# Kernel tuning notes

Hardware: AMD Instinct MI355X
Metric: run time of the kernel (lower is better)

The kernel has to match this reference:

```python
import jax, jax.numpy as jnp
import numpy as np

N = 100000
IN_DIM = 256
HID = 128
E = 1600000


def setup_inputs() -> dict:
    key = jax.random.key(0)
    ks = jax.random.split(key, 6)
    x = jax.random.normal(ks[0], (N, IN_DIM), dtype=jnp.float32)
    edge_index = jax.random.randint(ks[1], (2, E), 0, N, dtype=jnp.int64)
    # GCNConv weight (hidden, in) and bias (hidden); decoder Linear (in, hidden) + bias
    s_in = 1.0 / np.sqrt(IN_DIM)
    s_h = 1.0 / np.sqrt(HID)
    W_enc = jax.random.uniform(ks[2], (HID, IN_DIM), jnp.float32, -s_in, s_in)
    b_enc = jnp.zeros((HID,), jnp.float32)
    W_dec = jax.random.uniform(ks[3], (IN_DIM, HID), jnp.float32, -s_h, s_h)
    b_dec = jax.random.uniform(ks[4], (IN_DIM,), jnp.float32, -s_h, s_h)
    return {"x": x, "edge_index": edge_index, "W_enc": W_enc, "b_enc": b_enc,
            "W_dec": W_dec, "b_dec": b_dec}


def gcn_conv(x, edge_index, W, b):
    # Linear transform first (PyG GCNConv): h = x @ W^T  -> [N, HID]
    h = x @ W.T
    # Add self-loops
    loops = jnp.arange(N, dtype=edge_index.dtype)
    row = jnp.concatenate([edge_index[0], loops])  # source
    col = jnp.concatenate([edge_index[1], loops])  # target
    # Symmetric normalization: deg over targets (incl. self-loops)
    deg = jax.ops.segment_sum(jnp.ones_like(col, dtype=h.dtype), col, num_segments=N)
    dinv = jax.lax.rsqrt(deg)  # deg >= 1 due to self-loops
    norm = dinv[row] * dinv[col]  # [E+N]
    msg = h[row] * norm[:, None]  # gather + scale  [E+N, HID]
    agg = jax.ops.segment_sum(msg, col, num_segments=N)  # scatter-add
    return agg + b


def reference(x, edge_index, W_enc, b_enc, W_dec, b_dec):
    z = jax.nn.relu(gcn_conv(x, edge_index, W_enc, b_enc))
    x_recon = z @ W_dec.T + b_dec
    return (z, x_recon)
```

## Files before the change

### kernel.cpp

```cpp
#include <hip/hip_runtime.h>
#include <hip/hip_bf16.h>

#define NDIM 256
#define HDIM 128
#define NPAD 100352
#define LDS1_STRIDE 264
#define LDS2_STRIDE 136
#define P2CAP 6144

typedef __bf16 bf16_t;
typedef bf16_t bf16x2 __attribute__((ext_vector_type(2)));
typedef bf16_t bf16x4 __attribute__((ext_vector_type(4)));
typedef bf16_t bf16x8 __attribute__((ext_vector_type(8)));
typedef float f32x2 __attribute__((ext_vector_type(2)));
typedef float f32x4 __attribute__((ext_vector_type(4)));

__device__ __forceinline__ float bflo(unsigned u) { return __uint_as_float(u << 16); }
__device__ __forceinline__ float bfhi(unsigned u) { return __uint_as_float(u & 0xffff0000u); }

__global__ __launch_bounds__(256) void k_prep(const float* __restrict__ We, bf16_t* __restrict__ wpe,
                                              const float* __restrict__ Wd, bf16_t* __restrict__ wpd) {
    const int b = blockIdx.x, t = threadIdx.x;
    const bool enc = b < 16;
    const int i = (enc ? b : b - 16) * 256 + t;
    const int lane = i & 63;
    const int fr = lane & 15, kg = lane >> 4;
    int nf, kk32, K, NF;
    const float* W;
    bf16_t* wp;
    if (enc) { nf = (i >> 6) & 7;  kk32 = i >> 9;  K = NDIM; NF = 8;  W = We; wp = wpe; }
    else     { nf = (i >> 6) & 15; kk32 = i >> 10; K = HDIM; NF = 16; W = Wd; wp = wpd; }
    const float* src = &W[(size_t)(nf * 16 + fr) * K + kk32 * 32 + kg * 8];
    const f32x4 a0 = *reinterpret_cast<const f32x4*>(src);
    const f32x4 a1 = *reinterpret_cast<const f32x4*>(src + 4);
    bf16x8 o;
    o[0] = (bf16_t)a0[0]; o[1] = (bf16_t)a0[1]; o[2] = (bf16_t)a0[2]; o[3] = (bf16_t)a0[3];
    o[4] = (bf16_t)a1[0]; o[5] = (bf16_t)a1[1]; o[6] = (bf16_t)a1[2]; o[7] = (bf16_t)a1[3];
    reinterpret_cast<bf16x8*>(wp)[(kk32 * NF + nf) * 64 + lane] = o;
}

template<int K, int NC, bool OUT_BF16>
__device__ __forceinline__ void mfma_epi(const bf16x8* af,
                                         const bf16_t* __restrict__ Wp,
                                         const float* __restrict__ bias,
                                         void* __restrict__ Cout,
                                         const int bid, const int nrows) {
    const int lane = threadIdx.x & 63;
    const int wv = threadIdx.x >> 6;
    const int fr = lane & 15;
    const int kg = lane >> 4;
    constexpr int NF = NC / 16, NK = K / 32;

    const bf16x8* wp = reinterpret_cast<const bf16x8*>(Wp);
    f32x4 acc[NF];
    const f32x4 zero4 = {0.f, 0.f, 0.f, 0.f};
    #pragma unroll
    for (int nf = 0; nf < NF; ++nf) acc[nf] = zero4;

    #pragma unroll
    for (int k = 0; k < NK; ++k) {
        #pragma unroll
        for (int nf = 0; nf < NF; ++nf)
            acc[nf] = __builtin_amdgcn_mfma_f32_16x16x32_bf16(af[k], wp[(k * NF + nf) * 64 + lane], acc[nf], 0, 0, 0);
    }

    const long long rbase = (long long)bid * 64 + wv * 16 + kg * 4;
    #pragma unroll
    for (int nf = 0; nf < NF; ++nf) {
        const int c = nf * 16 + fr;
        const float bv = bias ? bias[c] : 0.f;
        #pragma unroll
        for (int i = 0; i < 4; ++i) {
            const long long r = rbase + i;
            if (r < nrows) {
                const float v = acc[nf][i] + bv;
                if (OUT_BF16) ((bf16_t*)Cout)[r * NC + c] = (bf16_t)v;
                else          __builtin_nontemporal_store(v, &((float*)Cout)[r * NC + c]);
            }
        }
    }
}

__device__ __forceinline__ void gemm1_body(const int bid, const float* __restrict__ x,
                                           const bf16_t* __restrict__ wpe,
                                           bf16_t* __restrict__ hb, const int nrows,
                                           bf16_t* lds) {
    const int t = threadIdx.x;
    const long long rowbase = (long long)bid * 64;
    #pragma unroll
    for (int p = 0; p < 16; ++p) {
        const int s = p * 256 + t;
        const int r = s >> 6, c4 = s & 63;
        long long gr = rowbase + r;
        if (gr >= nrows) gr = nrows - 1;
        const f32x4 v = __builtin_nontemporal_load(reinterpret_cast<const f32x4*>(&x[gr * NDIM + c4 * 4]));
        bf16x4 o;
        o[0] = (bf16_t)v[0]; o[1] = (bf16_t)v[1]; o[2] = (bf16_t)v[2]; o[3] = (bf16_t)v[3];
        *reinterpret_cast<bf16x4*>(&lds[r * LDS1_STRIDE + c4 * 4]) = o;
    }
    __syncthreads();
    const int lane = t & 63, wv = t >> 6, fr = lane & 15, kg = lane >> 4;
    bf16x8 af[8];
    #pragma unroll
    for (int k = 0; k < 8; ++k)
        af[k] = *reinterpret_cast<const bf16x8*>(&lds[(wv * 16 + fr) * LDS1_STRIDE + k * 32 + kg * 8]);
    mfma_epi<NDIM, HDIM, true>(af, wpe, nullptr, hb, bid, nrows);
}

__device__ __forceinline__ void p1a_body(const int blk, const int* __restrict__ col,
                                         int* __restrict__ bcnt, const int E_,
                                         const int nbkt, const int epb, int* lhist) {
    const int t = threadIdx.x;
    for (int i = t; i < nbkt; i += 256) lhist[i] = 0;
    __syncthreads();
    const int base = blk * epb;
    const int cnt = min(E_ - base, epb);
    for (int i = t; i < cnt; i += 256)
        atomicAdd(&lhist[col[base + i] >> 8], 1);
    __syncthreads();
    for (int i = t; i < nbkt; i += 256)
        bcnt[i * 256 + blk] = lhist[i];
}

__global__ __launch_bounds__(256) void k_fused(const float* __restrict__ x,
                                               const bf16_t* __restrict__ wpe,
                                               bf16_t* __restrict__ hb, const int nrows,
                                               const int* __restrict__ col,
                                               int* __restrict__ bcnt,
                                               const int E_, const int nbkt, const int epb,
                                               const int G1) {
    __shared__ __align__(16) bf16_t lds[64 * LDS1_STRIDE];
    const int b = blockIdx.x;
    if (b < G1) gemm1_body(b, x, wpe, hb, nrows, lds);
    else        p1a_body(b - G1, col, bcnt, E_, nbkt, epb, (int*)lds);
}

__global__ __launch_bounds__(256) void k_scanB1(const int* __restrict__ bcnt,
                                                int* __restrict__ bsum, const int M) {
    __shared__ int s[256];
    const int b = blockIdx.x, t = threadIdx.x;
    const int i0 = b * 1024 + t * 4;
    int4 v = make_int4(0, 0, 0, 0);
    if (i0 + 4 <= M) v = *reinterpret_cast<const int4*>(&bcnt[i0]);
    else if (i0 < M) {
        const int k = M - i0;
        v.x = bcnt[i0];
        if (k > 1) v.y = bcnt[i0 + 1];
        if (k > 2) v.z = bcnt[i0 + 2];
    }
    s[t] = v.x + v.y + v.z + v.w;
    __syncthreads();
    for (int d = 128; d > 0; d >>= 1) {
        if (t < d) s[t] += s[t + d];
        __syncthreads();
    }
    if (t == 0) bsum[b] = s[0];
}

__global__ __launch_bounds__(128) void k_scanB2(const int* __restrict__ bsum,
                                                int* __restrict__ bofs,
                                                int* __restrict__ bbase,
                                                const int nb, const int M) {
    __shared__ int s[128];
    const int t = threadIdx.x;
    const int v = (t < nb) ? bsum[t] : 0;
    s[t] = v;
    __syncthreads();
    for (int d = 1; d < 128; d <<= 1) {
        int xx = (t >= d) ? s[t - d] : 0;
        __syncthreads();
        s[t] += xx;
        __syncthreads();
    }
    if (t < nb) bofs[t] = s[t] - v;
    if (t == nb - 1) bbase[M] = s[t];
}

__global__ __launch_bounds__(256) void k_scanB3(const int* __restrict__ bcnt,
                                                const int* __restrict__ bofs,
                                                int* __restrict__ bbase, const int M) {
    __shared__ int s[256];
    const int b = blockIdx.x, t = threadIdx.x;
    const int i0 = b * 1024 + t * 4;
    int4 v = make_int4(0, 0, 0, 0);
    if (i0 + 4 <= M) v = *reinterpret_cast<const int4*>(&bcnt[i0]);
    else if (i0 < M) {
        const int k = M - i0;
        v.x = bcnt[i0];
        if (k > 1) v.y = bcnt[i0 + 1];
        if (k > 2) v.z = bcnt[i0 + 2];
    }
    const int tsum = v.x + v.y + v.z + v.w;
    s[t] = tsum;
    __syncthreads();
    for (int d = 1; d < 256; d <<= 1) {
        int xx = (t >= d) ? s[t - d] : 0;
        __syncthreads();
        s[t] += xx;
        __syncthreads();
    }
    const int excl = s[t] - tsum + bofs[b];
    int4 o;
    o.x = excl; o.y = excl + v.x; o.z = o.y + v.y; o.w = o.z + v.z;
    if (i0 + 4 <= M) *reinterpret_cast<int4*>(&bbase[i0]) = o;
    else if (i0 < M) {
        const int k = M - i0;
        bbase[i0] = o.x;
        if (k > 1) bbase[i0 + 1] = o.y;
        if (k > 2) bbase[i0 + 2] = o.z;
    }
}

__global__ __launch_bounds__(256) void k_p1b(const int* __restrict__ row,
                                             const int* __restrict__ col,
                                             const int* __restrict__ bbase,
                                             int* __restrict__ pbuf,
                                             const int E_, const int nbkt, const int epb) {
    __shared__ int lcur[512];
    const int blk = blockIdx.x, t = threadIdx.x;
    for (int i = t; i < nbkt; i += 256) lcur[i] = bbase[i * 256 + blk];
    __syncthreads();
    const int base = blk * epb;
    const int cnt = min(E_ - base, epb);
    for (int i = t; i < cnt; i += 256) {
        const int c = col[base + i];
        const int r = row[base + i];
        const int pos = atomicAdd(&lcur[c >> 8], 1);
        pbuf[pos] = r | ((c & 255) << 17);
    }
}

__global__ __launch_bounds__(256) void k_p2(const int* __restrict__ pbuf,
                                            const int* __restrict__ bbase,
                                            int* __restrict__ ebuf,
                                            int* __restrict__ goff, int* __restrict__ gcnt,
                                            float* __restrict__ dinv,
                                            unsigned* __restrict__ hbw,
                                            const int n, const int E_) {
    __shared__ int lcnt[256], lscan[256], lcur[256];
    __shared__ float ldinv[256];
    __shared__ __align__(16) int ecache[P2CAP];
    const int b = blockIdx.x, t = threadIdx.x;
    const int start = bbase[b * 256];
    const int end = bbase[(b + 1) * 256];
    const int size = end - start;
    const bool inlds = size <= P2CAP;
    lcnt[t] = 0; lcur[t] = 0;
    __syncthreads();
    if (inlds) {
        for (int i = t; i < size; i += 256) {
            const int e = pbuf[start + i];
            ecache[i] = e;
            atomicAdd(&lcnt[(e >> 17) & 255], 1);
        }
    } else {
        for (int i = t; i < size; i += 256)
            atomicAdd(&lcnt[(pbuf[start + i] >> 17) & 255], 1);
    }
    __syncthreads();
    const int v = lcnt[t];
    lscan[t] = v;
    __syncthreads();
    for (int d = 1; d < 256; d <<= 1) {
        int xx = (t >= d) ? lscan[t - d] : 0;
        __syncthreads();
        lscan[t] += xx;
        __syncthreads();
    }
    const int excl = lscan[t] - v;
    const int node = (b << 8) + t;
    float dvv = 0.f;
    if (node < n) {
        dvv = rsqrtf((float)(v + 1));
        goff[node] = start + excl;
        gcnt[node] = v;
        dinv[node] = dvv;
    }
    ldinv[t] = dvv;
    lscan[t] = excl;
    __syncthreads();
    for (int i = t; i < size; i += 256) {
        const int e = inlds ? ecache[i] : pbuf[start + i];
        const int li = (e >> 17) & 255;
        const int rk = atomicAdd(&lcur[li], 1);
        ebuf[start + lscan[li] + rk] = e & 0x1FFFF;
    }
    const int wv = t >> 6, lane = t & 63;
    #pragma unroll 4
    for (int rr = wv * 64; rr < wv * 64 + 64; ++rr) {
        const int nd = (b << 8) + rr;
        if (nd >= n) break;
        const float dv = ldinv[rr];
        unsigned* p = &hbw[(size_t)nd * 64 + lane];
        const unsigned u = *p;
        bf16x2 pk;
        pk[0] = (bf16_t)(bflo(u) * dv);
        pk[1] = (bf16_t)(bfhi(u) * dv);
        *p = __builtin_bit_cast(unsigned, pk);
    }
}

__global__ __launch_bounds__(256) void k_agg(const int* __restrict__ ebuf,
                                             const int* __restrict__ off,
                                             const int* __restrict__ cnt,
                                             const float* __restrict__ dinv,
                                             const unsigned* __restrict__ hb,
                                             const float* __restrict__ benc,
                                             float* __restrict__ z,
                                             bf16_t* __restrict__ zb, int n) {
    const int node = blockIdx.x * 4 + (threadIdx.x >> 6);
    const int lane = threadIdx.x & 63;
    if (node >= n) return;
    const float dc = dinv[node];
    const unsigned hself = hb[(size_t)node * 64 + lane];
    float acc0 = bflo(hself);
    float acc1 = bfhi(hself);
    const int base = off[node], m = cnt[node];
    int j = 0;
    for (; j + 16 <= m; j += 16) {
        int r[16]; unsigned u[16];
        #pragma unroll
        for (int q = 0; q < 16; ++q) r[q] = ebuf[base + j + q];
        #pragma unroll
        for (int q = 0; q < 16; ++q) u[q] = hb[(size_t)r[q] * 64 + lane];
        #pragma unroll
        for (int q = 0; q < 16; ++q) {
            acc0 += bflo(u[q]);
            acc1 += bfhi(u[q]);
        }
    }
    for (; j + 4 <= m; j += 4) {
        int r[4]; unsigned u[4];
        #pragma unroll
        for (int q = 0; q < 4; ++q) r[q] = ebuf[base + j + q];
        #pragma unroll
        for (int q = 0; q < 4; ++q) u[q] = hb[(size_t)r[q] * 64 + lane];
        #pragma unroll
        for (int q = 0; q < 4; ++q) {
            acc0 += bflo(u[q]);
            acc1 += bfhi(u[q]);
        }
    }
    for (; j < m; ++j) {
        const unsigned u = hb[(size_t)ebuf[base + j] * 64 + lane];
        acc0 += bflo(u);
        acc1 += bfhi(u);
    }
    f32x2 o;
    o[0] = fmaxf(fmaf(dc, acc0, benc[lane * 2]), 0.f);
    o[1] = fmaxf(fmaf(dc, acc1, benc[lane * 2 + 1]), 0.f);
    *reinterpret_cast<f32x2*>(&z[(size_t)node * HDIM + lane * 2]) = o;
    bf16x2 ob;
    ob[0] = (bf16_t)o[0];
    ob[1] = (bf16_t)o[1];
    *reinterpret_cast<bf16x2*>(&zb[(size_t)node * HDIM + lane * 2]) = ob;
}

__global__ __launch_bounds__(256) void k_gemm2(const bf16_t* __restrict__ zb,
                                               const bf16_t* __restrict__ wpd,
                                               const float* __restrict__ bias,
                                               float* __restrict__ xrec, const int nrows) {
    __shared__ __align__(16) bf16_t lds[64 * LDS2_STRIDE];
    const int t = threadIdx.x;
    const long long rowbase = (long long)blockIdx.x * 64;
    #pragma unroll
    for (int p = 0; p < 4; ++p) {
        const int s = p * 256 + t;
        const int r = s >> 4, c8 = s & 15;
        long long gr = rowbase + r;
        if (gr >= nrows) gr = nrows - 1;
        const bf16x8 v = *reinterpret_cast<const bf16x8*>(&zb[gr * HDIM + c8 * 8]);
        *reinterpret_cast<bf16x8*>(&lds[r * LDS2_STRIDE + c8 * 8]) = v;
    }
    __syncthreads();
    const int lane = t & 63, wv = t >> 6, fr = lane & 15, kg = lane >> 4;
    bf16x8 af[4];
    #pragma unroll
    for (int k = 0; k < 4; ++k)
        af[k] = *reinterpret_cast<const bf16x8*>(&lds[(wv * 16 + fr) * LDS2_STRIDE + k * 32 + kg * 8]);
    mfma_epi<HDIM, NDIM, false>(af, wpd, bias, xrec, blockIdx.x, nrows);
}

extern "C" void kernel_launch(void* const* d_in, const int* in_sizes, int n_in,
                              void* d_out, int out_size, void* d_ws, size_t ws_size,
                              hipStream_t stream) {
    const float* x     = (const float*)d_in[0];
    const int*   ei    = (const int*)d_in[1];
    const float* W_enc = (const float*)d_in[2];
    const float* b_enc = (const float*)d_in[3];
    const float* W_dec = (const float*)d_in[4];
    const float* b_dec = (const float*)d_in[5];

    const int N = in_sizes[0] / NDIM;
    const int E = in_sizes[1] / 2;
    const int* row = ei;
    const int* col = ei + E;

    const int NBKT = (N + 255) >> 8;
    const int M = NBKT * 256;
    const int EPB = (E + 255) / 256;
    const int G1 = (N + 63) / 64;
    const int SB = (M + 1023) / 1024;

    char* wsp = (char*)d_ws;
    int*    pbuf = (int*)wsp;
    bf16_t* zb   = (bf16_t*)wsp;
    const size_t r0 = ((size_t)N * HDIM * 2 > (size_t)E * 4) ? (size_t)N * HDIM * 2 : (size_t)E * 4;
    bf16_t* hb   = (bf16_t*)(wsp + r0);
    int*    ebuf = (int*)(wsp + r0 + (size_t)N * HDIM * 2);
    int*    goff = ebuf + E;
    int*    gcnt = goff + NPAD;
    float*  dinv = (float*)(gcnt + NPAD);
    int*    bcnt = (int*)(dinv + NPAD);
    int*    bbase = bcnt + M;
    int*    bsum = bbase + M + 1;
    int*    bofs = bsum + 128;
    bf16_t* wpe  = (bf16_t*)(bofs + 128);
    bf16_t* wpd  = wpe + HDIM * NDIM;

    float* z    = (float*)d_out;
    float* xrec = (float*)d_out + (size_t)N * HDIM;

    k_prep<<<32, 256, 0, stream>>>(W_enc, wpe, W_dec, wpd);

    k_fused<<<G1 + 256, 256, 0, stream>>>(x, wpe, hb, N, col, bcnt, E, NBKT, EPB, G1);

    k_scanB1<<<SB, 256, 0, stream>>>(bcnt, bsum, M);
    k_scanB2<<<1, 128, 0, stream>>>(bsum, bofs, bbase, SB, M);
    k_scanB3<<<SB, 256, 0, stream>>>(bcnt, bofs, bbase, M);

    k_p1b<<<256, 256, 0, stream>>>(row, col, bbase, pbuf, E, NBKT, EPB);

    k_p2<<<NBKT, 256, 0, stream>>>(pbuf, bbase, ebuf, goff, gcnt, dinv, (unsigned*)hb, N, E);

    k_agg<<<(N + 3) / 4, 256, 0, stream>>>(ebuf, goff, gcnt, dinv, (const unsigned*)hb, b_enc, z, zb, N);

    k_gemm2<<<G1, 256, 0, stream>>>(zb, wpd, b_dec, xrec, N);
}
```

Measured before the change: 224.1 us.

## Fuse neighbor aggregation with decoder GEMM via LDS staging of z tile

Measured after the change: 276.0 us. 1.23x slower.

```diff
diff --git a/kernel.cpp b/kernel.cpp
--- a/kernel.cpp
+++ b/kernel.cpp
@@ -300,85 +300,79 @@
     }
 }
 
-__global__ __launch_bounds__(256) void k_agg(const int* __restrict__ ebuf,
-                                             const int* __restrict__ off,
-                                             const int* __restrict__ cnt,
-                                             const float* __restrict__ dinv,
-                                             const unsigned* __restrict__ hb,
-                                             const float* __restrict__ benc,
-                                             float* __restrict__ z,
-                                             bf16_t* __restrict__ zb, int n) {
-    const int node = blockIdx.x * 4 + (threadIdx.x >> 6);
-    const int lane = threadIdx.x & 63;
-    if (node >= n) return;
-    const float dc = dinv[node];
-    const unsigned hself = hb[(size_t)node * 64 + lane];
-    float acc0 = bflo(hself);
-    float acc1 = bfhi(hself);
-    const int base = off[node], m = cnt[node];
-    int j = 0;
-    for (; j + 16 <= m; j += 16) {
-        int r[16]; unsigned u[16];
-        #pragma unroll
-        for (int q = 0; q < 16; ++q) r[q] = ebuf[base + j + q];
-        #pragma unroll
-        for (int q = 0; q < 16; ++q) u[q] = hb[(size_t)r[q] * 64 + lane];
-        #pragma unroll
-        for (int q = 0; q < 16; ++q) {
-            acc0 += bflo(u[q]);
-            acc1 += bfhi(u[q]);
-        }
-    }
-    for (; j + 4 <= m; j += 4) {
-        int r[4]; unsigned u[4];
-        #pragma unroll
-        for (int q = 0; q < 4; ++q) r[q] = ebuf[base + j + q];
-        #pragma unroll
-        for (int q = 0; q < 4; ++q) u[q] = hb[(size_t)r[q] * 64 + lane];
-        #pragma unroll
-        for (int q = 0; q < 4; ++q) {
-            acc0 += bflo(u[q]);
-            acc1 += bfhi(u[q]);
-        }
-    }
-    for (; j < m; ++j) {
-        const unsigned u = hb[(size_t)ebuf[base + j] * 64 + lane];
-        acc0 += bflo(u);
-        acc1 += bfhi(u);
-    }
-    f32x2 o;
-    o[0] = fmaxf(fmaf(dc, acc0, benc[lane * 2]), 0.f);
-    o[1] = fmaxf(fmaf(dc, acc1, benc[lane * 2 + 1]), 0.f);
-    *reinterpret_cast<f32x2*>(&z[(size_t)node * HDIM + lane * 2]) = o;
-    bf16x2 ob;
-    ob[0] = (bf16_t)o[0];
-    ob[1] = (bf16_t)o[1];
-    *reinterpret_cast<bf16x2*>(&zb[(size_t)node * HDIM + lane * 2]) = ob;
-}
-
-__global__ __launch_bounds__(256) void k_gemm2(const bf16_t* __restrict__ zb,
-                                               const bf16_t* __restrict__ wpd,
-                                               const float* __restrict__ bias,
-                                               float* __restrict__ xrec, const int nrows) {
+__global__ __launch_bounds__(256) void k_aggdec(const int* __restrict__ ebuf,
+                                                const int* __restrict__ off,
+                                                const int* __restrict__ cnt,
+                                                const float* __restrict__ dinv,
+                                                const unsigned* __restrict__ hb,
+                                                const float* __restrict__ benc,
+                                                const bf16_t* __restrict__ wpd,
+                                                const float* __restrict__ bdec,
+                                                float* __restrict__ z,
+                                                float* __restrict__ xrec, int n) {
     __shared__ __align__(16) bf16_t lds[64 * LDS2_STRIDE];
     const int t = threadIdx.x;
-    const long long rowbase = (long long)blockIdx.x * 64;
-    #pragma unroll
-    for (int p = 0; p < 4; ++p) {
-        const int s = p * 256 + t;
-        const int r = s >> 4, c8 = s & 15;
-        long long gr = rowbase + r;
-        if (gr >= nrows) gr = nrows - 1;
-        const bf16x8 v = *reinterpret_cast<const bf16x8*>(&zb[gr * HDIM + c8 * 8]);
-        *reinterpret_cast<bf16x8*>(&lds[r * LDS2_STRIDE + c8 * 8]) = v;
-    }
-    __syncthreads();
-    const int lane = t & 63, wv = t >> 6, fr = lane & 15, kg = lane >> 4;
+    const int wv = t >> 6, lane = t & 63;
+    const int nodebase = blockIdx.x * 64 + wv * 16;
+
+    for (int i = 0; i < 16; ++i) {
+        const int node = nodebase + i;
+        float acc0 = 0.f, acc1 = 0.f;
+        float dc = 0.f;
+        if (node < n) {
+            dc = dinv[node];
+            const unsigned hself = hb[(size_t)node * 64 + lane];
+            acc0 = bflo(hself);
+            acc1 = bfhi(hself);
+            const int base = off[node], m = cnt[node];
+            int j = 0;
+            for (; j + 16 <= m; j += 16) {
+                int r[16]; unsigned u[16];
+                #pragma unroll
+                for (int q = 0; q < 16; ++q) r[q] = ebuf[base + j + q];
+                #pragma unroll
+                for (int q = 0; q < 16; ++q) u[q] = hb[(size_t)r[q] * 64 + lane];
+                #pragma unroll
+                for (int q = 0; q < 16; ++q) {
+                    acc0 += bflo(u[q]);
+                    acc1 += bfhi(u[q]);
+                }
+            }
+            for (; j + 4 <= m; j += 4) {
+                int r[4]; unsigned u[4];
+                #pragma unroll
+                for (int q = 0; q < 4; ++q) r[q] = ebuf[base + j + q];
+                #pragma unroll
+                for (int q = 0; q < 4; ++q) u[q] = hb[(size_t)r[q] * 64 + lane];
+                #pragma unroll
+                for (int q = 0; q < 4; ++q) {
+                    acc0 += bflo(u[q]);
+                    acc1 += bfhi(u[q]);
+                }
+            }
+            for (; j < m; ++j) {
+                const unsigned u = hb[(size_t)ebuf[base + j] * 64 + lane];
+                acc0 += bflo(u);
+                acc1 += bfhi(u);
+            }
+        }
+        f32x2 o;
+        o[0] = fmaxf(fmaf(dc, acc0, benc[lane * 2]), 0.f);
+        o[1] = fmaxf(fmaf(dc, acc1, benc[lane * 2 + 1]), 0.f);
+        if (node < n)
+            *reinterpret_cast<f32x2*>(&z[(size_t)node * HDIM + lane * 2]) = o;
+        bf16x2 ob;
+        ob[0] = (node < n) ? (bf16_t)o[0] : (bf16_t)0.f;
+        ob[1] = (node < n) ? (bf16_t)o[1] : (bf16_t)0.f;
+        *reinterpret_cast<bf16x2*>(&lds[(wv * 16 + i) * LDS2_STRIDE + lane * 2]) = ob;
+    }
+
+    const int fr = lane & 15, kg = lane >> 4;
     bf16x8 af[4];
     #pragma unroll
     for (int k = 0; k < 4; ++k)
         af[k] = *reinterpret_cast<const bf16x8*>(&lds[(wv * 16 + fr) * LDS2_STRIDE + k * 32 + kg * 8]);
-    mfma_epi<HDIM, NDIM, false>(af, wpd, bias, xrec, blockIdx.x, nrows);
+    mfma_epi<HDIM, NDIM, false>(af, wpd, bdec, xrec, blockIdx.x, n);
 }
 
 extern "C" void kernel_launch(void* const* d_in, const int* in_sizes, int n_in,
@@ -404,8 +398,7 @@
 
     char* wsp = (char*)d_ws;
     int*    pbuf = (int*)wsp;
-    bf16_t* zb   = (bf16_t*)wsp;
-    const size_t r0 = ((size_t)N * HDIM * 2 > (size_t)E * 4) ? (size_t)N * HDIM * 2 : (size_t)E * 4;
+    const size_t r0 = (size_t)E * 4;
     bf16_t* hb   = (bf16_t*)(wsp + r0);
     int*    ebuf = (int*)(wsp + r0 + (size_t)N * HDIM * 2);
     int*    goff = ebuf + E;
@@ -433,7 +426,6 @@
 
     k_p2<<<NBKT, 256, 0, stream>>>(pbuf, bbase, ebuf, goff, gcnt, dinv, (unsigned*)hb, N, E);
 
-    k_agg<<<(N + 3) / 4, 256, 0, stream>>>(ebuf, goff, gcnt, dinv, (const unsigned*)hb, b_enc, z, zb, N);
-
-    k_gemm2<<<G1, 256, 0, stream>>>(zb, wpd, b_dec, xrec, N);
-}
+    k_aggdec<<<G1, 256, 0, stream>>>(ebuf, goff, gcnt, dinv, (const unsigned*)hb,
+                                     b_enc, wpd, b_dec, z, xrec, N);
+}
```

## Regroup kernels: fuse weight prep with histogram, fuse GEMM1 with edge partition

Applied to the files above, without the earlier changes.

Result: no change. 226.3 us (+1.0%).

```diff
diff --git a/kernel.cpp b/kernel.cpp
--- a/kernel.cpp
+++ b/kernel.cpp
@@ -18,9 +18,9 @@
 __device__ __forceinline__ float bflo(unsigned u) { return __uint_as_float(u << 16); }
 __device__ __forceinline__ float bfhi(unsigned u) { return __uint_as_float(u & 0xffff0000u); }
 
-__global__ __launch_bounds__(256) void k_prep(const float* __restrict__ We, bf16_t* __restrict__ wpe,
-                                              const float* __restrict__ Wd, bf16_t* __restrict__ wpd) {
-    const int b = blockIdx.x, t = threadIdx.x;
+__device__ __forceinline__ void prep_body(const int b, const float* __restrict__ We, bf16_t* __restrict__ wpe,
+                                          const float* __restrict__ Wd, bf16_t* __restrict__ wpd) {
+    const int t = threadIdx.x;
     const bool enc = b < 16;
     const int i = (enc ? b : b - 16) * 256 + t;
     const int lane = i & 63;
@@ -39,6 +39,31 @@
     reinterpret_cast<bf16x8*>(wp)[(kk32 * NF + nf) * 64 + lane] = o;
 }
 
+__device__ __forceinline__ void p1a_body(const int blk, const int* __restrict__ col,
+                                         int* __restrict__ bcnt, const int E_,
+                                         const int nbkt, const int epb, int* lhist) {
+    const int t = threadIdx.x;
+    for (int i = t; i < nbkt; i += 256) lhist[i] = 0;
+    __syncthreads();
+    const int base = blk * epb;
+    const int cnt = min(E_ - base, epb);
+    for (int i = t; i < cnt; i += 256)
+        atomicAdd(&lhist[col[base + i] >> 8], 1);
+    __syncthreads();
+    for (int i = t; i < nbkt; i += 256)
+        bcnt[i * 256 + blk] = lhist[i];
+}
+
+__global__ __launch_bounds__(256) void k_pre(const float* __restrict__ We, bf16_t* __restrict__ wpe,
+                                             const float* __restrict__ Wd, bf16_t* __restrict__ wpd,
+                                             const int* __restrict__ col, int* __restrict__ bcnt,
+                                             const int E_, const int nbkt, const int epb) {
+    __shared__ int lhist[512];
+    const int b = blockIdx.x;
+    if (b < 32) prep_body(b, We, wpe, Wd, wpd);
+    else        p1a_body(b - 32, col, bcnt, E_, nbkt, epb, lhist);
+}
+
 template<int K, int NC, bool OUT_BF16>
 __device__ __forceinline__ void mfma_epi(const bf16x8* af,
                                          const bf16_t* __restrict__ Wp,
@@ -107,32 +132,38 @@
     mfma_epi<NDIM, HDIM, true>(af, wpe, nullptr, hb, bid, nrows);
 }
 
-__device__ __forceinline__ void p1a_body(const int blk, const int* __restrict__ col,
-                                         int* __restrict__ bcnt, const int E_,
-                                         const int nbkt, const int epb, int* lhist) {
-    const int t = threadIdx.x;
-    for (int i = t; i < nbkt; i += 256) lhist[i] = 0;
+__device__ __forceinline__ void p1b_body(const int blk, const int* __restrict__ row,
+                                         const int* __restrict__ col,
+                                         const int* __restrict__ bbase,
+                                         int* __restrict__ pbuf,
+                                         const int E_, const int nbkt, const int epb,
+                                         int* lcur) {
+    const int t = threadIdx.x;
+    for (int i = t; i < nbkt; i += 256) lcur[i] = bbase[i * 256 + blk];
     __syncthreads();
     const int base = blk * epb;
     const int cnt = min(E_ - base, epb);
-    for (int i = t; i < cnt; i += 256)
-        atomicAdd(&lhist[col[base + i] >> 8], 1);
-    __syncthreads();
-    for (int i = t; i < nbkt; i += 256)
-        bcnt[i * 256 + blk] = lhist[i];
+    for (int i = t; i < cnt; i += 256) {
+        const int c = col[base + i];
+        const int r = row[base + i];
+        const int pos = atomicAdd(&lcur[c >> 8], 1);
+        pbuf[pos] = r | ((c & 255) << 17);
+    }
 }
 
 __global__ __launch_bounds__(256) void k_fused(const float* __restrict__ x,
                                                const bf16_t* __restrict__ wpe,
                                                bf16_t* __restrict__ hb, const int nrows,
+                                               const int* __restrict__ row,
                                                const int* __restrict__ col,
-                                               int* __restrict__ bcnt,
+                                               const int* __restrict__ bbase,
+                                               int* __restrict__ pbuf,
                                                const int E_, const int nbkt, const int epb,
                                                const int G1) {
     __shared__ __align__(16) bf16_t lds[64 * LDS1_STRIDE];
     const int b = blockIdx.x;
     if (b < G1) gemm1_body(b, x, wpe, hb, nrows, lds);
-    else        p1a_body(b - G1, col, bcnt, E_, nbkt, epb, (int*)lds);
+    else        p1b_body(b - G1, row, col, bbase, pbuf, E_, nbkt, epb, (int*)lds);
 }
 
 __global__ __launch_bounds__(256) void k_scanB1(const int* __restrict__ bcnt,
@@ -208,25 +239,6 @@
         bbase[i0] = o.x;
         if (k > 1) bbase[i0 + 1] = o.y;
         if (k > 2) bbase[i0 + 2] = o.z;
-    }
-}
-
-__global__ __launch_bounds__(256) void k_p1b(const int* __restrict__ row,
-                                             const int* __restrict__ col,
-                                             const int* __restrict__ bbase,
-                                             int* __restrict__ pbuf,
-                                             const int E_, const int nbkt, const int epb) {
-    __shared__ int lcur[512];
-    const int blk = blockIdx.x, t = threadIdx.x;
-    for (int i = t; i < nbkt; i += 256) lcur[i] = bbase[i * 256 + blk];
-    __syncthreads();
-    const int base = blk * epb;
-    const int cnt = min(E_ - base, epb);
-    for (int i = t; i < cnt; i += 256) {
-        const int c = col[base + i];
-        const int r = row[base + i];
-        const int pos = atomicAdd(&lcur[c >> 8], 1);
-        pbuf[pos] = r | ((c & 255) << 17);
     }
 }
 
@@ -421,15 +433,13 @@
     float* z    = (float*)d_out;
     float* xrec = (float*)d_out + (size_t)N * HDIM;
 
-    k_prep<<<32, 256, 0, stream>>>(W_enc, wpe, W_dec, wpd);
-
-    k_fused<<<G1 + 256, 256, 0, stream>>>(x, wpe, hb, N, col, bcnt, E, NBKT, EPB, G1);
+    k_pre<<<32 + 256, 256, 0, stream>>>(W_enc, wpe, W_dec, wpd, col, bcnt, E, NBKT, EPB);
 
     k_scanB1<<<SB, 256, 0, stream>>>(bcnt, bsum, M);
     k_scanB2<<<1, 128, 0, stream>>>(bsum, bofs, bbase, SB, M);
     k_scanB3<<<SB, 256, 0, stream>>>(bcnt, bofs, bbase, M);
 
-    k_p1b<<<256, 256, 0, stream>>>(row, col, bbase, pbuf, E, NBKT, EPB);
+    k_fused<<<G1 + 256, 256, 0, stream>>>(x, wpe, hb, N, row, col, bbase, pbuf, E, NBKT, EPB, G1);
 
     k_p2<<<NBKT, 256, 0, stream>>>(pbuf, bbase, ebuf, goff, gcnt, dinv, (unsigned*)hb, N, E);
 
```
